# Optimization experiments

Measured on AMD Instinct MI355X. Metric: run time of the kernel, lower is better.

## Reference

```python
import jax, jax.numpy as jnp
import numpy as np

BATCH, TIME, IN, HID = 32, 512, 512, 1024
THRESHOLD = 1.0
BETA = 1.0 / 2.0  # 1/tau


def setup_inputs() -> dict:
    key = jax.random.key(0)
    kx, kw, kb = jax.random.split(key, 3)
    x = jax.random.normal(kx, (BATCH, TIME, IN), dtype=jnp.float32)
    bound = 1.0 / np.sqrt(IN)  # nn.Linear default init range
    W = jax.random.uniform(kw, (HID, IN), minval=-bound, maxval=bound, dtype=jnp.float32)
    b = jax.random.uniform(kb, (HID,), minval=-bound, maxval=bound, dtype=jnp.float32)
    return {"x": x, "W": W, "b": b}


def reference(x, W, b):
    # Precompute all per-step linear projections in one big GEMM: [B,T,H]
    hidden = jnp.einsum("bti,hi->bth", x, W) + b

    def step(mem, h_t):
        # h_t: [B,H]
        mem = BETA * mem + h_t
        spk = (mem > THRESHOLD).astype(h_t.dtype)
        mem = mem * (1.0 - spk)  # hard reset
        return mem, spk

    mem0 = jnp.zeros((x.shape[0], W.shape[0]), dtype=x.dtype)
    # scan over time: [T,B,H]
    _, spikes = jax.lax.scan(step, mem0, jnp.swapaxes(hidden, 0, 1))
    return jnp.swapaxes(spikes, 0, 1)  # [B,T,H]
```

## Files before the change

### kernel.cpp

```cpp
#include <hip/hip_runtime.h>

#define BATCH 32
#define TIME  512
#define INF   512
#define HIDF  1024

#define MBT  256
#define NBH  128
#define KCH  16
#define NCH  (INF / KCH)
#define XTILEF (MBT * KCH)
#define WTILEF (NBH * KCH)

#define GLD16(g, l) __builtin_amdgcn_global_load_lds(                      \
    (const __attribute__((address_space(1))) void*)(g),                    \
    (__attribute__((address_space(3))) void*)(l), 16, 0, 0)

__global__ __launch_bounds__(256, 2)
void snn_gemm_seqfma(const float* __restrict__ x, const float* __restrict__ W,
                     const float* __restrict__ bias, float* __restrict__ hidden) {
    __shared__ __align__(16) float xs[2 * XTILEF];
    __shared__ __align__(16) float ws[2 * WTILEF];

    const int tid = threadIdx.x;
    const int l   = tid & 63;
    const int wv  = __builtin_amdgcn_readfirstlane(tid >> 6);
    const int lx  = l & 7;
    const int ly  = (l >> 3) & 7;
    const int bt0 = blockIdx.y * MBT;
    const int h0  = blockIdx.x * NBH;
    const int wbt = 128 * (wv >> 1);
    const int wh  = 64 * (wv & 1);

    const int rl = l >> 2;
    const int qs = (l & 3) ^ ((rl >> 1) & 3);
    const float* xg0 = x + (size_t)(bt0 + 64 * wv + rl) * INF + qs * 4;
    const float* wg0 = W + (size_t)(h0 + 32 * wv + rl) * INF + qs * 4;
    const int xOff = (64 * wv) * KCH;
    const int wOff = (32 * wv) * KCH;

    GLD16(xg0,            xs + xOff);
    GLD16(xg0 + 16 * INF, xs + xOff + 256);
    GLD16(xg0 + 32 * INF, xs + xOff + 512);
    GLD16(xg0 + 48 * INF, xs + xOff + 768);
    GLD16(wg0,            ws + wOff);
    GLD16(wg0 + 16 * INF, ws + wOff + 256);

    float acc[16][8];
    #pragma unroll
    for (int r = 0; r < 16; ++r)
        #pragma unroll
        for (int c = 0; c < 8; ++c) acc[r][c] = 0.0f;

    const int keyx = (ly >> 1) & 3;
    const int keyw = (lx >> 1) & 3;

    __syncthreads();

    for (int kc = 0; kc < NCH; ++kc) {
        const int p  = kc & 1;
        const int np = p ^ 1;

        if (kc + 1 < NCH) {
            const int so = (kc + 1) * KCH;
            float* xd = xs + np * XTILEF;
            float* wd = ws + np * WTILEF;
            GLD16(xg0 + so,            xd + xOff);
            GLD16(xg0 + so + 16 * INF, xd + xOff + 256);
            GLD16(xg0 + so + 32 * INF, xd + xOff + 512);
            GLD16(xg0 + so + 48 * INF, xd + xOff + 768);
            GLD16(wg0 + so,            wd + wOff);
            GLD16(wg0 + so + 16 * INF, wd + wOff + 256);
        }

        const float* xrow = xs + p * XTILEF + (wbt + ly) * KCH;
        const float* wrow = ws + p * WTILEF + (wh  + lx) * KCH;
        #pragma unroll
        for (int g = 0; g < 4; ++g) {
            const float* xg_ = xrow + (g ^ keyx) * 4;
            const float* wg_ = wrow + (g ^ keyw) * 4;
            float4 wf[8];
            #pragma unroll
            for (int c = 0; c < 8; ++c)
                wf[c] = *(const float4*)(wg_ + c * 8 * KCH);
            #pragma unroll
            for (int r = 0; r < 16; ++r) {
                float4 xf = *(const float4*)(xg_ + r * 8 * KCH);
                #pragma unroll
                for (int c = 0; c < 8; ++c)
                    acc[r][c] = __fmaf_rn(xf.x, wf[c].x, acc[r][c]);
                #pragma unroll
                for (int c = 0; c < 8; ++c)
                    acc[r][c] = __fmaf_rn(xf.y, wf[c].y, acc[r][c]);
                #pragma unroll
                for (int c = 0; c < 8; ++c)
                    acc[r][c] = __fmaf_rn(xf.z, wf[c].z, acc[r][c]);
                #pragma unroll
                for (int c = 0; c < 8; ++c)
                    acc[r][c] = __fmaf_rn(xf.w, wf[c].w, acc[r][c]);
            }
        }
        __syncthreads();
    }

    float bv[8];
    #pragma unroll
    for (int c = 0; c < 8; ++c) bv[c] = bias[h0 + wh + lx + 8 * c];
    #pragma unroll
    for (int r = 0; r < 16; ++r) {
        float* orow = hidden + (size_t)(bt0 + wbt + ly + 8 * r) * HIDF
                             + h0 + wh + lx;
        #pragma unroll
        for (int c = 0; c < 8; ++c)
            orow[8 * c] = __fadd_rn(acc[r][c], bv[c]);
    }
}

__global__ __launch_bounds__(64)
void snn_scan_np(float* __restrict__ io) {
    const int n  = blockIdx.x * 64 + threadIdx.x;
    const int b  = n >> 9;
    const int h2 = n & 511;
    float2* p = (float2*)io + (size_t)b * TIME * 512 + h2;

    float m0 = 0.0f, m1 = 0.0f;
    for (int tb = 0; tb < TIME / 32; ++tb) {
        float2 v[32];
        #pragma unroll
        for (int u = 0; u < 32; ++u) v[u] = p[(size_t)(tb * 32 + u) * 512];
        #pragma unroll
        for (int u = 0; u < 32; ++u) {
            m0 = __fadd_rn(__fmul_rn(0.5f, m0), v[u].x);
            m1 = __fadd_rn(__fmul_rn(0.5f, m1), v[u].y);
            bool s0 = m0 > 1.0f, s1 = m1 > 1.0f;
            v[u].x = s0 ? 1.0f : 0.0f;
            v[u].y = s1 ? 1.0f : 0.0f;
            if (s0) m0 = 0.0f;
            if (s1) m1 = 0.0f;
        }
        #pragma unroll
        for (int u = 0; u < 32; ++u) p[(size_t)(tb * 32 + u) * 512] = v[u];
    }
}

extern "C" void kernel_launch(void* const* d_in, const int* in_sizes, int n_in,
                              void* d_out, int out_size, void* d_ws, size_t ws_size,
                              hipStream_t stream) {
    const float* x    = (const float*)d_in[0];
    const float* W    = (const float*)d_in[1];
    const float* bias = (const float*)d_in[2];
    float* out = (float*)d_out;

    dim3 g1(HIDF / NBH, (BATCH * TIME) / MBT);
    snn_gemm_seqfma<<<g1, 256, 0, stream>>>(x, W, bias, out);

    snn_scan_np<<<(BATCH * HIDF / 2) / 64, 64, 0, stream>>>(out);
}
```

Before: 335.1 us.

## Fuse GEMM and membrane scan into one kernel with per-batch full-time tiles

Merges the projection GEMM and the LIF scan into one kernel. Each block now owns one batch element and 64 hidden units across all 512 time steps, so the scan runs in registers after the GEMM and the carry is handed between threads through shared memory in 32 serialized steps. This removes the write and re-read of the hidden tensor and the second kernel launch. The cost is a serialized scan phase in which only 8 of 256 threads work at each step, plus a larger shared-memory X tile (double-buffered 512x16 floats) that may limit occupancy.

```diff
diff --git a/kernel.cpp b/kernel.cpp
--- a/kernel.cpp
+++ b/kernel.cpp
@@ -5,46 +5,59 @@
 #define INF   512
 #define HIDF  1024
 
-#define MBT  256
-#define NBH  128
-#define KCH  16
-#define NCH  (INF / KCH)
-#define XTILEF (MBT * KCH)
-#define WTILEF (NBH * KCH)
+#define KCH   16
+#define NCH   (INF / KCH)
+#define XTILE (TIME * KCH)
+#define WTILE (64 * KCH)
 
 #define GLD16(g, l) __builtin_amdgcn_global_load_lds(                      \
     (const __attribute__((address_space(1))) void*)(g),                    \
     (__attribute__((address_space(3))) void*)(l), 16, 0, 0)
 
 __global__ __launch_bounds__(256, 2)
-void snn_gemm_seqfma(const float* __restrict__ x, const float* __restrict__ W,
-                     const float* __restrict__ bias, float* __restrict__ hidden) {
-    __shared__ __align__(16) float xs[2 * XTILEF];
-    __shared__ __align__(16) float ws[2 * WTILEF];
+void snn_fused(const float* __restrict__ x, const float* __restrict__ W,
+               const float* __restrict__ bias, float* __restrict__ out) {
+    __shared__ __align__(16) float xs[2 * XTILE];
+    __shared__ __align__(16) float ws[2 * WTILE];
+    __shared__ float carry[64];
 
     const int tid = threadIdx.x;
     const int l   = tid & 63;
     const int wv  = __builtin_amdgcn_readfirstlane(tid >> 6);
     const int lx  = l & 7;
     const int ly  = (l >> 3) & 7;
-    const int bt0 = blockIdx.y * MBT;
-    const int h0  = blockIdx.x * NBH;
-    const int wbt = 128 * (wv >> 1);
-    const int wh  = 64 * (wv & 1);
+    const int ty  = wv * 8 + ly;
+    const int b   = blockIdx.y;
+    const int h0  = blockIdx.x * 64;
+
+    const float* xb_g = x + (size_t)b * TIME * INF;
 
     const int rl = l >> 2;
-    const int qs = (l & 3) ^ ((rl >> 1) & 3);
-    const float* xg0 = x + (size_t)(bt0 + 64 * wv + rl) * INF + qs * 4;
-    const float* wg0 = W + (size_t)(h0 + 32 * wv + rl) * INF + qs * 4;
-    const int xOff = (64 * wv) * KCH;
-    const int wOff = (32 * wv) * KCH;
+    const float* xsrc[8];
+    #pragma unroll
+    for (int i = 0; i < 8; ++i) {
+        const int row = 128 * wv + 16 * i + rl;
+        const int q   = (l & 3) ^ ((row >> 4) & 3) ^ ((row >> 1) & 3);
+        xsrc[i] = xb_g + (size_t)row * INF + q * 4;
+    }
+    const int wrow = 16 * wv + rl;
+    const int wq   = (l & 3) ^ ((wrow >> 3) & 3) ^ ((wrow >> 1) & 3);
+    const float* wsrc = W + (size_t)(h0 + wrow) * INF + wq * 4;
 
-    GLD16(xg0,            xs + xOff);
-    GLD16(xg0 + 16 * INF, xs + xOff + 256);
-    GLD16(xg0 + 32 * INF, xs + xOff + 512);
-    GLD16(xg0 + 48 * INF, xs + xOff + 768);
-    GLD16(wg0,            ws + wOff);
-    GLD16(wg0 + 16 * INF, ws + wOff + 256);
+    const int tyq = ty & 3, lxq = lx & 3;
+    int xoff[2][4], woff[2][4];
+    #pragma unroll
+    for (int p2 = 0; p2 < 2; ++p2)
+        #pragma unroll
+        for (int q = 0; q < 4; ++q) {
+            xoff[p2][q] = p2 * XTILE + ty * 256 + (tyq ^ q) * 4;
+            woff[p2][q] = p2 * WTILE + lx * 128 + (lxq ^ q) * 4;
+        }
+
+    #pragma unroll
+    for (int i = 0; i < 8; ++i)
+        GLD16(xsrc[i], xs + wv * 2048 + i * 256);
+    GLD16(wsrc, ws + wv * 256);
 
     float acc[16][8];
     #pragma unroll
@@ -52,52 +65,35 @@
         #pragma unroll
         for (int c = 0; c < 8; ++c) acc[r][c] = 0.0f;
 
-    const int keyx = (ly >> 1) & 3;
-    const int keyw = (lx >> 1) & 3;
-
     __syncthreads();
 
     for (int kc = 0; kc < NCH; ++kc) {
         const int p  = kc & 1;
         const int np = p ^ 1;
-
         if (kc + 1 < NCH) {
             const int so = (kc + 1) * KCH;
-            float* xd = xs + np * XTILEF;
-            float* wd = ws + np * WTILEF;
-            GLD16(xg0 + so,            xd + xOff);
-            GLD16(xg0 + so + 16 * INF, xd + xOff + 256);
-            GLD16(xg0 + so + 32 * INF, xd + xOff + 512);
-            GLD16(xg0 + so + 48 * INF, xd + xOff + 768);
-            GLD16(wg0 + so,            wd + wOff);
-            GLD16(wg0 + so + 16 * INF, wd + wOff + 256);
+            #pragma unroll
+            for (int i = 0; i < 8; ++i)
+                GLD16(xsrc[i] + so, xs + np * XTILE + wv * 2048 + i * 256);
+            GLD16(wsrc + so, ws + np * WTILE + wv * 256);
         }
-
-        const float* xrow = xs + p * XTILEF + (wbt + ly) * KCH;
-        const float* wrow = ws + p * WTILEF + (wh  + lx) * KCH;
         #pragma unroll
         for (int g = 0; g < 4; ++g) {
-            const float* xg_ = xrow + (g ^ keyx) * 4;
-            const float* wg_ = wrow + (g ^ keyw) * 4;
             float4 wf[8];
             #pragma unroll
             for (int c = 0; c < 8; ++c)
-                wf[c] = *(const float4*)(wg_ + c * 8 * KCH);
+                wf[c] = *(const float4*)(ws + woff[p][g ^ ((c >> 1) & 3)] + c * 16);
             #pragma unroll
             for (int r = 0; r < 16; ++r) {
-                float4 xf = *(const float4*)(xg_ + r * 8 * KCH);
+                float4 xv = *(const float4*)(xs + xoff[p][g ^ ((r >> 1) & 3)] + r * 16);
                 #pragma unroll
-                for (int c = 0; c < 8; ++c)
-                    acc[r][c] = __fmaf_rn(xf.x, wf[c].x, acc[r][c]);
+                for (int c = 0; c < 8; ++c) acc[r][c] = __fmaf_rn(xv.x, wf[c].x, acc[r][c]);
                 #pragma unroll
-                for (int c = 0; c < 8; ++c)
-                    acc[r][c] = __fmaf_rn(xf.y, wf[c].y, acc[r][c]);
+                for (int c = 0; c < 8; ++c) acc[r][c] = __fmaf_rn(xv.y, wf[c].y, acc[r][c]);
                 #pragma unroll
-                for (int c = 0; c < 8; ++c)
-                    acc[r][c] = __fmaf_rn(xf.z, wf[c].z, acc[r][c]);
+                for (int c = 0; c < 8; ++c) acc[r][c] = __fmaf_rn(xv.z, wf[c].z, acc[r][c]);
                 #pragma unroll
-                for (int c = 0; c < 8; ++c)
-                    acc[r][c] = __fmaf_rn(xf.w, wf[c].w, acc[r][c]);
+                for (int c = 0; c < 8; ++c) acc[r][c] = __fmaf_rn(xv.w, wf[c].w, acc[r][c]);
             }
         }
         __syncthreads();
@@ -105,41 +101,41 @@
 
     float bv[8];
     #pragma unroll
-    for (int c = 0; c < 8; ++c) bv[c] = bias[h0 + wh + lx + 8 * c];
+    for (int c = 0; c < 8; ++c) bv[c] = bias[h0 + lx * 8 + c];
+    #pragma unroll
+    for (int r = 0; r < 16; ++r)
+        #pragma unroll
+        for (int c = 0; c < 8; ++c) acc[r][c] = __fadd_rn(acc[r][c], bv[c]);
+
+    for (int step = 0; step < 32; ++step) {
+        __syncthreads();
+        if (ty == step) {
+            float m[8];
+            #pragma unroll
+            for (int c = 0; c < 8; ++c)
+                m[c] = (step == 0) ? 0.0f : carry[lx * 8 + c];
+            #pragma unroll
+            for (int r = 0; r < 16; ++r) {
+                #pragma unroll
+                for (int c = 0; c < 8; ++c) {
+                    m[c] = __fadd_rn(__fmul_rn(0.5f, m[c]), acc[r][c]);
+                    const bool s = m[c] > 1.0f;
+                    acc[r][c] = s ? 1.0f : 0.0f;
+                    if (s) m[c] = 0.0f;
+                }
+            }
+            #pragma unroll
+            for (int c = 0; c < 8; ++c) carry[lx * 8 + c] = m[c];
+        }
+    }
+
     #pragma unroll
     for (int r = 0; r < 16; ++r) {
-        float* orow = hidden + (size_t)(bt0 + wbt + ly + 8 * r) * HIDF
-                             + h0 + wh + lx;
-        #pragma unroll
-        for (int c = 0; c < 8; ++c)
-            orow[8 * c] = __fadd_rn(acc[r][c], bv[c]);
-    }
-}
-
-__global__ __launch_bounds__(64)
-void snn_scan_np(float* __restrict__ io) {
-    const int n  = blockIdx.x * 64 + threadIdx.x;
-    const int b  = n >> 9;
-    const int h2 = n & 511;
-    float2* p = (float2*)io + (size_t)b * TIME * 512 + h2;
-
-    float m0 = 0.0f, m1 = 0.0f;
-    for (int tb = 0; tb < TIME / 32; ++tb) {
-        float2 v[32];
-        #pragma unroll
-        for (int u = 0; u < 32; ++u) v[u] = p[(size_t)(tb * 32 + u) * 512];
-        #pragma unroll
-        for (int u = 0; u < 32; ++u) {
-            m0 = __fadd_rn(__fmul_rn(0.5f, m0), v[u].x);
-            m1 = __fadd_rn(__fmul_rn(0.5f, m1), v[u].y);
-            bool s0 = m0 > 1.0f, s1 = m1 > 1.0f;
-            v[u].x = s0 ? 1.0f : 0.0f;
-            v[u].y = s1 ? 1.0f : 0.0f;
-            if (s0) m0 = 0.0f;
-            if (s1) m1 = 0.0f;
-        }
-        #pragma unroll
-        for (int u = 0; u < 32; ++u) p[(size_t)(tb * 32 + u) * 512] = v[u];
+        float* orow = out + (size_t)(b * TIME + ty * 16 + r) * HIDF + h0 + lx * 8;
+        float4 o0 = {acc[r][0], acc[r][1], acc[r][2], acc[r][3]};
+        float4 o1 = {acc[r][4], acc[r][5], acc[r][6], acc[r][7]};
+        ((float4*)orow)[0] = o0;
+        ((float4*)orow)[1] = o1;
     }
 }
 
@@ -151,8 +147,6 @@
     const float* bias = (const float*)d_in[2];
     float* out = (float*)d_out;
 
-    dim3 g1(HIDF / NBH, (BATCH * TIME) / MBT);
-    snn_gemm_seqfma<<<g1, 256, 0, stream>>>(x, W, bias, out);
-
-    snn_scan_np<<<(BATCH * HIDF / 2) / 64, 64, 0, stream>>>(out);
+    dim3 grid(HIDF / 64, BATCH);
+    snn_fused<<<grid, 256, 0, stream>>>(x, W, bias, out);
 }
```

Measured after the change: 523.9 us. 56.4% more time.
